# Kernel optimization log

Hardware: AMD Instinct MI355X
Metric: run time of the kernel (lower is better)

## Reference

```python
import jax, jax.numpy as jnp
import numpy as np

B, RATIO, IN_CH, H = 32, 32, 64, 8
E = IN_CH * H                 # embed_dim = in_channels * n_heads = 512
NODES_PER_GRAPH = 512
N = B * NODES_PER_GRAPH       # 16384 source nodes


def setup_inputs() -> dict:
    key = jax.random.key(0)
    ks = jax.random.split(key, 6)
    x = jax.random.normal(ks[0], (N, E), dtype=jnp.float32)
    # edge_index is accepted by forward but unused in 'attn' mode
    edge_index = jax.random.randint(ks[1], (2, 262144), 0, N, dtype=jnp.int32)
    # per-node graph id, sorted, equal-size graphs (batch[-1] + 1 == B)
    batch = jnp.repeat(jnp.arange(B, dtype=jnp.int32), NODES_PER_GRAPH)
    # learned params: cluster query seeds + MultiheadAttention in/out projections
    xcent_base = jax.random.normal(ks[2], (RATIO, E), dtype=jnp.float32)
    in_proj_w = jax.random.normal(ks[3], (3 * E, E), dtype=jnp.float32) / np.sqrt(E).astype(np.float32)
    in_proj_b = jnp.zeros((3 * E,), dtype=jnp.float32)
    out_proj_w = jax.random.normal(ks[4], (E, E), dtype=jnp.float32) / np.sqrt(E).astype(np.float32)
    out_proj_b = jnp.zeros((E,), dtype=jnp.float32)
    return dict(x=x, edge_index=edge_index, batch=batch, xcent_base=xcent_base,
                in_proj_w=in_proj_w, in_proj_b=in_proj_b,
                out_proj_w=out_proj_w, out_proj_b=out_proj_b)


def reference(x, edge_index, batch, xcent_base, in_proj_w, in_proj_b, out_proj_w, out_proj_b):
    # BipartPool.forward, mode='attn':
    #   x_aggrs = xcent_base.repeat(batch_size, 1)  -> queries [L, E], L = B*ratio
    #   MultiheadAttention(q=x_aggrs, k=v=x, attn_mask=mask[batch].T)
    # mask[batch].T is True (disallowed) where query's graph != node's graph.
    L = B * RATIO
    head_dim = E // H
    x_aggrs = jnp.tile(xcent_base, (B, 1))                        # [L, E]

    wq, wk, wv = jnp.split(in_proj_w, 3, axis=0)                  # each [E, E]
    bq, bk, bv = jnp.split(in_proj_b, 3, axis=0)
    q = (x_aggrs @ wq.T + bq).reshape(L, H, head_dim).transpose(1, 0, 2)  # [H, L, hd]
    k = (x @ wk.T + bk).reshape(N, H, head_dim).transpose(1, 0, 2)        # [H, N, hd]
    v = (x @ wv.T + bv).reshape(N, H, head_dim).transpose(1, 0, 2)        # [H, N, hd]

    batchcent = jnp.repeat(jnp.arange(B, dtype=batch.dtype), RATIO)       # [L]
    allowed = batchcent[:, None] == batch[None, :]                        # [L, N]

    scale = np.float32(1.0 / np.sqrt(head_dim))
    scores = jnp.einsum('hld,hnd->hln', q, k) * scale                     # [H, L, N]
    scores = jnp.where(allowed[None], scores, -jnp.inf)
    attn = jax.nn.softmax(scores, axis=-1)
    out = jnp.einsum('hln,hnd->hld', attn, v)                             # [H, L, hd]
    out = out.transpose(1, 0, 2).reshape(L, E)
    xcent = out @ out_proj_w.T + out_proj_b                               # [L, E]
    # original returns (xcent.reshape(B, ratio, E), None, None, batchcent, None, None)
    return xcent.reshape(B, RATIO, E), batchcent
```

## Files before the change

kernel.cpp:

```cpp
#include <hip/hip_runtime.h>
#include <hip/hip_bf16.h>

#define NGRAPH 32
#define NHEAD 8
#define EMB 512
#define NNODES 16384
#define NPG 512
#define LQ 1024
#define PST 520

typedef __attribute__((ext_vector_type(8))) short short8;
typedef __attribute__((ext_vector_type(4))) float f32x4;

static __device__ __forceinline__ unsigned short f2bf(float f) {
  union { float f; unsigned u; } v; v.f = f;
  unsigned r = (v.u + 0x7fffu + ((v.u >> 16) & 1u)) >> 16;
  return (unsigned short)r;
}

static __device__ __forceinline__ void gload_lds16(const ushort* g, ushort* l) {
  __builtin_amdgcn_global_load_lds(
      (const __attribute__((address_space(1))) unsigned*)g,
      (__attribute__((address_space(3))) unsigned*)l, 16, 0, 0);
}

#define BARRIER_LGKM()                                        \
  do {                                                        \
    asm volatile("s_waitcnt lgkmcnt(0)" ::: "memory");        \
    __builtin_amdgcn_s_barrier();                             \
  } while (0)

__global__ __launch_bounds__(256) void prep_x(const float* __restrict__ x,
                                              ushort* __restrict__ xb,
                                              ushort* __restrict__ xbT) {
  __shared__ ushort tile[64][68];
  int id = blockIdx.x;
  int xr = id & 7, j = id >> 3;
  int m = j >> 6, r = j & 63;
  int g = xr + 8 * m;
  int bc = r & 7;
  int br = g * 8 + (r >> 3);
  int t = threadIdx.x;
  int trr = t >> 4, tc = t & 15;
#pragma unroll
  for (int p = 0; p < 4; ++p) {
    int n = trr + p * 16;
    long gi = (long)(br * 64 + n) * EMB + bc * 64 + tc * 4;
    float4 v = *reinterpret_cast<const float4*>(x + gi);
    ushort4 o;
    o.x = f2bf(v.x); o.y = f2bf(v.y); o.z = f2bf(v.z); o.w = f2bf(v.w);
    *reinterpret_cast<ushort4*>(xb + gi) = o;
    *reinterpret_cast<ushort4*>(&tile[n][tc * 4]) = o;
  }
  __syncthreads();
#pragma unroll
  for (int p = 0; p < 4; ++p) {
    int e = trr + p * 16;
    int n0 = tc * 4;
    ushort4 o;
    o.x = tile[n0][e]; o.y = tile[n0 + 1][e];
    o.z = tile[n0 + 2][e]; o.w = tile[n0 + 3][e];
    *reinterpret_cast<ushort4*>(xbT + (long)(bc * 64 + e) * NNODES + br * 64 + n0) = o;
  }
}

__global__ void prep_wb(const float* __restrict__ wv, const float* __restrict__ wo,
                        const float* __restrict__ wq, const float* __restrict__ xc,
                        const float* __restrict__ wk,
                        ushort* __restrict__ wvb, ushort* __restrict__ wob,
                        ushort* __restrict__ wqb, ushort* __restrict__ xcb,
                        ushort* __restrict__ wkT, float* __restrict__ bcent) {
  __shared__ ushort tile[32][33];
  int b = blockIdx.x;
  if (b == 784) {
    int i = threadIdx.x;
#pragma unroll
    for (int p = 0; p < 4; ++p) bcent[i + p * 256] = (float)((i + p * 256) >> 5);
    return;
  }
  if (b >= 785) {
    int b2 = b - 785;
    int bd = b2 >> 4, bk = b2 & 15;
    int t = threadIdx.x, lr = t >> 5, lc = t & 31;
#pragma unroll
    for (int p = 0; p < 4; ++p) {
      int rr = lr + p * 8;
      tile[rr][lc] = f2bf(0.125f * wk[(long)(bd * 32 + rr) * EMB + bk * 32 + lc]);
    }
    __syncthreads();
#pragma unroll
    for (int p = 0; p < 4; ++p) {
      int rr = lr + p * 8;
      wkT[(long)(bk * 32 + rr) * EMB + bd * 32 + lc] = tile[lc][rr];
    }
    return;
  }
  const float* src; ushort* dst; int off;
  if (b < 256)       { src = wv; dst = wvb; off = b; }
  else if (b < 512)  { src = wo; dst = wob; off = b - 256; }
  else if (b < 768)  { src = wq; dst = wqb; off = b - 512; }
  else               { src = xc; dst = xcb; off = b - 768; }
  int i = (off * 256 + threadIdx.x) * 4;
  float4 v = *reinterpret_cast<const float4*>(src + i);
  ushort4 o;
  o.x = f2bf(v.x); o.y = f2bf(v.y); o.z = f2bf(v.z); o.w = f2bf(v.w);
  *reinterpret_cast<ushort4*>(dst + i) = o;
}

__global__ __launch_bounds__(256) void qpc_mfma(
    const ushort* __restrict__ xcb, const ushort* __restrict__ wqb,
    const float* __restrict__ bq, const ushort* __restrict__ wkTb,
    ushort* __restrict__ PCb) {
  __shared__ ushort Qs[32][72];
  int h = blockIdx.x >> 2, qs = blockIdx.x & 3;
  int t = threadIdx.x, w = t >> 6, lane = t & 63;
  int lr = lane & 15, grp = lane >> 4, ko = grp * 8;

  f32x4 qa[2];
  qa[0] = (f32x4)(0.0f); qa[1] = (f32x4)(0.0f);
#pragma unroll 4
  for (int kk = 0; kk < EMB; kk += 32) {
    short8 a0 = *reinterpret_cast<const short8*>(xcb + lr * EMB + kk + ko);
    short8 a1 = *reinterpret_cast<const short8*>(xcb + (16 + lr) * EMB + kk + ko);
    short8 b  = *reinterpret_cast<const short8*>(wqb + (long)(h * 64 + w * 16 + lr) * EMB + kk + ko);
    qa[0] = __builtin_amdgcn_mfma_f32_16x16x32_bf16(a0, b, qa[0], 0, 0, 0);
    qa[1] = __builtin_amdgcn_mfma_f32_16x16x32_bf16(a1, b, qa[1], 0, 0, 0);
  }
  float bias = bq[h * 64 + w * 16 + lr];
#pragma unroll
  for (int i = 0; i < 2; ++i)
#pragma unroll
    for (int r = 0; r < 4; ++r)
      Qs[i * 16 + grp * 4 + r][w * 16 + lr] = f2bf(qa[i][r] + bias);
  __syncthreads();

  f32x4 pa[2][2];
#pragma unroll
  for (int i = 0; i < 2; ++i)
#pragma unroll
    for (int j = 0; j < 2; ++j) pa[i][j] = (f32x4)(0.0f);
#pragma unroll
  for (int kk = 0; kk < 64; kk += 32) {
    short8 a0 = *reinterpret_cast<const short8*>(&Qs[lr][kk + ko]);
    short8 a1 = *reinterpret_cast<const short8*>(&Qs[16 + lr][kk + ko]);
#pragma unroll
    for (int j = 0; j < 2; ++j) {
      short8 b = *reinterpret_cast<const short8*>(
          wkTb + (long)(qs * 128 + w * 32 + j * 16 + lr) * EMB + h * 64 + kk + ko);
      pa[0][j] = __builtin_amdgcn_mfma_f32_16x16x32_bf16(a0, b, pa[0][j], 0, 0, 0);
      pa[1][j] = __builtin_amdgcn_mfma_f32_16x16x32_bf16(a1, b, pa[1][j], 0, 0, 0);
    }
  }
#pragma unroll
  for (int i = 0; i < 2; ++i)
#pragma unroll
    for (int j = 0; j < 2; ++j)
#pragma unroll
      for (int r = 0; r < 4; ++r)
        PCb[(long)(h * 32 + i * 16 + grp * 4 + r) * EMB + qs * 128 + w * 32 + j * 16 + lr] =
            f2bf(pa[i][j][r]);
}

__global__ __launch_bounds__(1024) void fused_attn(
    const ushort* __restrict__ PCb, const ushort* __restrict__ xb,
    const ushort* __restrict__ xbT, const ushort* __restrict__ wvb,
    const float* __restrict__ bvb, ushort* __restrict__ aout) {
  __shared__ ushort PCl[32 * PST];
  __shared__ ushort PBuf[32 * PST];
  __shared__ ushort Bbuf[2][16384];
  __shared__ float rmax[32][16];
  __shared__ float rsum[32][16];

  const int g = blockIdx.x & 31, h = blockIdx.x >> 5;
  const int t = threadIdx.x, w = t >> 6, lane = t & 63;
  const int lr = lane & 15, grp = lane >> 4;
  const int koU = grp * 8;

  const ushort* xg  = xb  + (long)g * NPG * EMB;
  const ushort* xTg = xbT + g * NPG;

  const int srow0 = w * 32 + (lane >> 2);
  const int spart = lane & 3;

  auto STAGE1 = [&](int c, int db) {
#pragma unroll
    for (int q = 0; q < 2; ++q) {
      int row = srow0 + q * 16;
      int psrc = spart ^ ((row >> 1) & 3);
      gload_lds16(xg + (long)row * EMB + c * 32 + psrc * 8,
                  &Bbuf[db][(w * 32 + q * 16) * 32]);
    }
  };
  auto STAGE3 = [&](int c, int db) {
#pragma unroll
    for (int q = 0; q < 2; ++q) {
      int row = srow0 + q * 16;
      int psrc = spart ^ ((row >> 1) & 3);
      gload_lds16(xTg + (long)row * NNODES + c * 32 + psrc * 8,
                  &Bbuf[db][(w * 32 + q * 16) * 32]);
    }
  };

  STAGE1(0, 0);
  STAGE1(1, 1);
  {
    const ushort* pc = PCb + h * 32 * EMB;
#pragma unroll
    for (int p = 0; p < 2; ++p) {
      int u = t + p * 1024;
      int row = u >> 6, col = (u & 63) * 8;
      *reinterpret_cast<short8*>(&PCl[row * PST + col]) =
          *reinterpret_cast<const short8*>(pc + row * EMB + col);
    }
  }
  BARRIER_LGKM();

  f32x4 acc[2][2];
#pragma unroll
  for (int i = 0; i < 2; ++i)
#pragma unroll
    for (int j = 0; j < 2; ++j) acc[i][j] = (f32x4)(0.0f);

#pragma unroll
  for (int c = 0; c < 16; ++c) {
    const int db = c & 1;
    asm volatile("s_waitcnt vmcnt(2)" ::: "memory");
    __builtin_amdgcn_sched_barrier(0);
    short8 a0 = *reinterpret_cast<const short8*>(&PCl[lr * PST + c * 32 + koU]);
    short8 a1 = *reinterpret_cast<const short8*>(&PCl[(16 + lr) * PST + c * 32 + koU]);
    short8 bv[2];
#pragma unroll
    for (int j = 0; j < 2; ++j) {
      int n = w * 32 + j * 16 + lr;
      int psrc = grp ^ ((n >> 1) & 3);
      bv[j] = *reinterpret_cast<const short8*>(&Bbuf[db][n * 32 + psrc * 8]);
    }
#pragma unroll
    for (int j = 0; j < 2; ++j) {
      acc[0][j] = __builtin_amdgcn_mfma_f32_16x16x32_bf16(a0, bv[j], acc[0][j], 0, 0, 0);
      acc[1][j] = __builtin_amdgcn_mfma_f32_16x16x32_bf16(a1, bv[j], acc[1][j], 0, 0, 0);
    }
    __builtin_amdgcn_sched_barrier(0);
    if (c < 14) STAGE1(c + 2, db);
    else        STAGE3(c - 14, db);
  }

#pragma unroll
  for (int i = 0; i < 2; ++i)
#pragma unroll
    for (int r = 0; r < 4; ++r) {
      float m = fmaxf(acc[i][0][r], acc[i][1][r]);
      m = fmaxf(m, __shfl_xor(m, 1)); m = fmaxf(m, __shfl_xor(m, 2));
      m = fmaxf(m, __shfl_xor(m, 4)); m = fmaxf(m, __shfl_xor(m, 8));
      if (lr == 0) rmax[i * 16 + grp * 4 + r][w] = m;
    }
  BARRIER_LGKM();
#pragma unroll
  for (int i = 0; i < 2; ++i)
#pragma unroll
    for (int r = 0; r < 4; ++r) {
      int row = i * 16 + grp * 4 + r;
      float m = rmax[row][0];
#pragma unroll
      for (int q = 1; q < 16; ++q) m = fmaxf(m, rmax[row][q]);
      float s = 0.f;
#pragma unroll
      for (int j = 0; j < 2; ++j) {
        float e = __expf(acc[i][j][r] - m);
        acc[i][j][r] = e;
        s += e;
      }
      s += __shfl_xor(s, 1); s += __shfl_xor(s, 2);
      s += __shfl_xor(s, 4); s += __shfl_xor(s, 8);
      if (lr == 0) rsum[row][w] = s;
    }
  BARRIER_LGKM();
#pragma unroll
  for (int i = 0; i < 2; ++i)
#pragma unroll
    for (int r = 0; r < 4; ++r) {
      int row = i * 16 + grp * 4 + r;
      float tot = rsum[row][0];
#pragma unroll
      for (int q = 1; q < 16; ++q) tot += rsum[row][q];
      float inv = 1.f / tot;
#pragma unroll
      for (int j = 0; j < 2; ++j)
        PBuf[row * PST + w * 32 + j * 16 + lr] = f2bf(acc[i][j][r] * inv);
    }
  BARRIER_LGKM();

  f32x4 acc2[2][2];
#pragma unroll
  for (int i = 0; i < 2; ++i)
#pragma unroll
    for (int j = 0; j < 2; ++j) acc2[i][j] = (f32x4)(0.0f);

#pragma unroll
  for (int c = 0; c < 16; ++c) {
    const int db = c & 1;
    if (c < 15) asm volatile("s_waitcnt vmcnt(2)" ::: "memory");
    else        asm volatile("s_waitcnt vmcnt(0)" ::: "memory");
    __builtin_amdgcn_sched_barrier(0);
    short8 a0 = *reinterpret_cast<const short8*>(&PBuf[lr * PST + c * 32 + koU]);
    short8 a1 = *reinterpret_cast<const short8*>(&PBuf[(16 + lr) * PST + c * 32 + koU]);
    short8 bv[2];
#pragma unroll
    for (int j = 0; j < 2; ++j) {
      int e = w * 32 + j * 16 + lr;
      int psrc = grp ^ ((e >> 1) & 3);
      bv[j] = *reinterpret_cast<const short8*>(&Bbuf[db][e * 32 + psrc * 8]);
    }
#pragma unroll
    for (int j = 0; j < 2; ++j) {
      acc2[0][j] = __builtin_amdgcn_mfma_f32_16x16x32_bf16(a0, bv[j], acc2[0][j], 0, 0, 0);
      acc2[1][j] = __builtin_amdgcn_mfma_f32_16x16x32_bf16(a1, bv[j], acc2[1][j], 0, 0, 0);
    }
    __builtin_amdgcn_sched_barrier(0);
    if (c < 14) STAGE3(c + 2, db);
  }
  BARRIER_LGKM();

#pragma unroll
  for (int i = 0; i < 2; ++i)
#pragma unroll
    for (int r = 0; r < 4; ++r) {
      int row = i * 16 + grp * 4 + r;
#pragma unroll
      for (int j = 0; j < 2; ++j)
        PBuf[row * PST + w * 32 + j * 16 + lr] = f2bf(acc2[i][j][r]);
    }
  BARRIER_LGKM();

  if (w < 8) {
    int wr = w >> 2, wc = w & 3;
    f32x4 acc3 = (f32x4)(0.0f);
    const ushort* wvh = wvb + (long)(h * 64 + wc * 16) * EMB;
#pragma unroll
    for (int c = 0; c < 16; ++c) {
      short8 a = *reinterpret_cast<const short8*>(&PBuf[(wr * 16 + lr) * PST + c * 32 + koU]);
      short8 b = *reinterpret_cast<const short8*>(wvh + (long)lr * EMB + c * 32 + koU);
      acc3 = __builtin_amdgcn_mfma_f32_16x16x32_bf16(a, b, acc3, 0, 0, 0);
    }
    float bias = bvb[h * 64 + wc * 16 + lr];
#pragma unroll
    for (int r = 0; r < 4; ++r) {
      int row = wr * 16 + grp * 4 + r;
      aout[(long)(g * 32 + row) * EMB + h * 64 + wc * 16 + lr] = f2bf(acc3[r] + bias);
    }
  }
}

template <int KK, int FM, int FN, int WM, int WN, bool OUT_BF16, bool HAS_BIAS>
__global__ void gemm_abt(const ushort* __restrict__ A, const ushort* __restrict__ Bm,
                         void* __restrict__ C, const float* __restrict__ bias,
                         int lda, int ldb, int ldc) {
  int tid = threadIdx.x;
  int wave = tid >> 6, lane = tid & 63;
  int wr = wave / WN, wc = wave % WN;
  int rowBase = blockIdx.y * (WM * FM * 16) + wr * FM * 16;
  int colBase = blockIdx.x * (WN * FN * 16) + wc * FN * 16;
  int lr = lane & 15;
  int ko = (lane >> 4) * 8;

  f32x4 acc[FM][FN];
#pragma unroll
  for (int i = 0; i < FM; ++i)
#pragma unroll
    for (int j = 0; j < FN; ++j) acc[i][j] = (f32x4)(0.0f);

#pragma unroll 8
  for (int kk = 0; kk < KK; kk += 32) {
    short8 av[FM], bv[FN];
#pragma unroll
    for (int i = 0; i < FM; ++i)
      av[i] = *reinterpret_cast<const short8*>(A + (long)(rowBase + i * 16 + lr) * lda + kk + ko);
#pragma unroll
    for (int j = 0; j < FN; ++j)
      bv[j] = *reinterpret_cast<const short8*>(Bm + (long)(colBase + j * 16 + lr) * ldb + kk + ko);
#pragma unroll
    for (int i = 0; i < FM; ++i)
#pragma unroll
      for (int j = 0; j < FN; ++j)
        acc[i][j] = __builtin_amdgcn_mfma_f32_16x16x32_bf16(av[i], bv[j], acc[i][j], 0, 0, 0);
  }

  int or0 = (lane >> 4) * 4;
#pragma unroll
  for (int i = 0; i < FM; ++i) {
#pragma unroll
    for (int j = 0; j < FN; ++j) {
      int col = colBase + j * 16 + lr;
      float bval = HAS_BIAS ? bias[col] : 0.f;
#pragma unroll
      for (int r = 0; r < 4; ++r) {
        int row = rowBase + i * 16 + or0 + r;
        float v = acc[i][j][r] + bval;
        if (OUT_BF16)
          ((ushort*)C)[(long)row * ldc + col] = f2bf(v);
        else
          ((float*)C)[(long)row * ldc + col] = v;
      }
    }
  }
}

extern "C" void kernel_launch(void* const* d_in, const int* in_sizes, int n_in,
                              void* d_out, int out_size, void* d_ws, size_t ws_size,
                              hipStream_t stream) {
  const float* x          = (const float*)d_in[0];
  const float* xcent_base = (const float*)d_in[3];
  const float* in_proj_w  = (const float*)d_in[4];
  const float* in_proj_b  = (const float*)d_in[5];
  const float* out_proj_w = (const float*)d_in[6];
  const float* out_proj_b = (const float*)d_in[7];

  char* w = (char*)d_ws;
  ushort* xb   = (ushort*)(w);
  ushort* xbT  = (ushort*)(w + 16777216);
  ushort* PCb  = (ushort*)(w + 33554432);
  ushort* wvb  = (ushort*)(w + 33816576);
  ushort* wob  = (ushort*)(w + 34340864);
  ushort* wqb  = (ushort*)(w + 34865152);
  ushort* wkTb = (ushort*)(w + 35389440);
  ushort* xcb  = (ushort*)(w + 35913728);
  ushort* aout = (ushort*)(w + 35946496);

  const float* wq = in_proj_w;
  const float* wk = in_proj_w + 512 * 512;
  const float* wv = in_proj_w + 1024 * 512;
  const float* bq = in_proj_b;
  const float* bv = in_proj_b + 1024;

  prep_x<<<2048, 256, 0, stream>>>(x, xb, xbT);
  prep_wb<<<1041, 256, 0, stream>>>(wv, out_proj_w, wq, xcent_base, wk,
                                    wvb, wob, wqb, xcb, wkTb,
                                    (float*)d_out + LQ * EMB);
  qpc_mfma<<<32, 256, 0, stream>>>(xcb, wqb, bq, wkTb, PCb);

  fused_attn<<<256, 1024, 0, stream>>>(PCb, xb, xbT, wvb, bv, aout);

  gemm_abt<512, 1, 2, 2, 2, false, true><<<dim3(8, 32, 1), 256, 0, stream>>>(
      aout, wob, d_out, out_proj_b, 512, 512, 512);
}
```

Baseline: 62.94 us.

## Fuse prep kernels and Q·Wk precompute; fold out-projection into attention via atomics

Merges the x conversion, weight conversion, batchcent fill and the Q/PC precompute into a single prep_all launch. The PC blocks now read fp32 weights directly, converting Wq and xcent inline and staging a transposed Wk slice in LDS. The separate out-projection GEMM is removed: each attention block multiplies its per-head output by the matching Wo slice and atomically adds into a zeroed fp32 output. This cuts launches and the aout round-trip, but adds a memset, fp32 atomics across 8 heads with non-deterministic summation order, and a serial tail in every attention block.

```diff
diff --git a/kernel.cpp b/kernel.cpp
--- a/kernel.cpp
+++ b/kernel.cpp
@@ -18,6 +18,13 @@
   return (unsigned short)r;
 }
 
+static __device__ __forceinline__ short8 cvt8(float4 a, float4 b) {
+  short8 r;
+  r[0] = f2bf(a.x); r[1] = f2bf(a.y); r[2] = f2bf(a.z); r[3] = f2bf(a.w);
+  r[4] = f2bf(b.x); r[5] = f2bf(b.y); r[6] = f2bf(b.z); r[7] = f2bf(b.w);
+  return r;
+}
+
 static __device__ __forceinline__ void gload_lds16(const ushort* g, ushort* l) {
   __builtin_amdgcn_global_load_lds(
       (const __attribute__((address_space(1))) unsigned*)g,
@@ -30,144 +37,151 @@
     __builtin_amdgcn_s_barrier();                             \
   } while (0)
 
-__global__ __launch_bounds__(256) void prep_x(const float* __restrict__ x,
-                                              ushort* __restrict__ xb,
-                                              ushort* __restrict__ xbT) {
-  __shared__ ushort tile[64][68];
-  int id = blockIdx.x;
-  int xr = id & 7, j = id >> 3;
-  int m = j >> 6, r = j & 63;
-  int g = xr + 8 * m;
-  int bc = r & 7;
-  int br = g * 8 + (r >> 3);
-  int t = threadIdx.x;
-  int trr = t >> 4, tc = t & 15;
-#pragma unroll
-  for (int p = 0; p < 4; ++p) {
-    int n = trr + p * 16;
-    long gi = (long)(br * 64 + n) * EMB + bc * 64 + tc * 4;
-    float4 v = *reinterpret_cast<const float4*>(x + gi);
+__global__ __launch_bounds__(256) void prep_all(
+    const float* __restrict__ x, const float* __restrict__ wv,
+    const float* __restrict__ wo, const float* __restrict__ wq,
+    const float* __restrict__ wk, const float* __restrict__ xc,
+    const float* __restrict__ bq,
+    ushort* __restrict__ xb, ushort* __restrict__ xbT,
+    ushort* __restrict__ wvb, ushort* __restrict__ wob,
+    ushort* __restrict__ PCb, float* __restrict__ bcent) {
+  __shared__ ushort smemU[11776];
+  const int b = blockIdx.x;
+  const int t = threadIdx.x;
+
+  if (b < 2048) {
+    ushort* tile = smemU;
+    int xr = b & 7, j = b >> 3;
+    int m = j >> 6, r = j & 63;
+    int g = xr + 8 * m;
+    int bc = r & 7;
+    int br = g * 8 + (r >> 3);
+    int trr = t >> 4, tc = t & 15;
+#pragma unroll
+    for (int p = 0; p < 4; ++p) {
+      int n = trr + p * 16;
+      long gi = (long)(br * 64 + n) * EMB + bc * 64 + tc * 4;
+      float4 v = *reinterpret_cast<const float4*>(x + gi);
+      ushort4 o;
+      o.x = f2bf(v.x); o.y = f2bf(v.y); o.z = f2bf(v.z); o.w = f2bf(v.w);
+      *reinterpret_cast<ushort4*>(xb + gi) = o;
+      *reinterpret_cast<ushort4*>(&tile[n * 68 + tc * 4]) = o;
+    }
+    __syncthreads();
+#pragma unroll
+    for (int p = 0; p < 4; ++p) {
+      int e = trr + p * 16;
+      int n0 = tc * 4;
+      ushort4 o;
+      o.x = tile[n0 * 68 + e];       o.y = tile[(n0 + 1) * 68 + e];
+      o.z = tile[(n0 + 2) * 68 + e]; o.w = tile[(n0 + 3) * 68 + e];
+      *reinterpret_cast<ushort4*>(xbT + (long)(bc * 64 + e) * NNODES + br * 64 + n0) = o;
+    }
+    return;
+  }
+
+  if (b < 2560) {
+    int off = b - 2048;
+    const float* src = (off < 256) ? wv : wo;
+    ushort* dst = (off < 256) ? wvb : wob;
+    off &= 255;
+    int i = (off * 256 + t) * 4;
+    float4 v = *reinterpret_cast<const float4*>(src + i);
     ushort4 o;
     o.x = f2bf(v.x); o.y = f2bf(v.y); o.z = f2bf(v.z); o.w = f2bf(v.w);
-    *reinterpret_cast<ushort4*>(xb + gi) = o;
-    *reinterpret_cast<ushort4*>(&tile[n][tc * 4]) = o;
-  }
-  __syncthreads();
-#pragma unroll
-  for (int p = 0; p < 4; ++p) {
-    int e = trr + p * 16;
-    int n0 = tc * 4;
-    ushort4 o;
-    o.x = tile[n0][e]; o.y = tile[n0 + 1][e];
-    o.z = tile[n0 + 2][e]; o.w = tile[n0 + 3][e];
-    *reinterpret_cast<ushort4*>(xbT + (long)(bc * 64 + e) * NNODES + br * 64 + n0) = o;
-  }
-}
-
-__global__ void prep_wb(const float* __restrict__ wv, const float* __restrict__ wo,
-                        const float* __restrict__ wq, const float* __restrict__ xc,
-                        const float* __restrict__ wk,
-                        ushort* __restrict__ wvb, ushort* __restrict__ wob,
-                        ushort* __restrict__ wqb, ushort* __restrict__ xcb,
-                        ushort* __restrict__ wkT, float* __restrict__ bcent) {
-  __shared__ ushort tile[32][33];
-  int b = blockIdx.x;
-  if (b == 784) {
-    int i = threadIdx.x;
-#pragma unroll
-    for (int p = 0; p < 4; ++p) bcent[i + p * 256] = (float)((i + p * 256) >> 5);
+    *reinterpret_cast<ushort4*>(dst + i) = o;
     return;
   }
-  if (b >= 785) {
-    int b2 = b - 785;
-    int bd = b2 >> 4, bk = b2 & 15;
-    int t = threadIdx.x, lr = t >> 5, lc = t & 31;
-#pragma unroll
-    for (int p = 0; p < 4; ++p) {
-      int rr = lr + p * 8;
-      tile[rr][lc] = f2bf(0.125f * wk[(long)(bd * 32 + rr) * EMB + bk * 32 + lc]);
-    }
+
+  if (b == 2560) {
+#pragma unroll
+    for (int p = 0; p < 4; ++p) bcent[t + p * 256] = (float)((t + p * 256) >> 5);
+    return;
+  }
+
+  {
+    ushort* Qs  = smemU;
+    ushort* WkT = smemU + 2304;
+    int qb = b - 2561;
+    int h = qb >> 2, qs = qb & 3;
+    int w = t >> 6, lane = t & 63;
+    int lr = lane & 15, grp = lane >> 4, ko = grp * 8;
+
+    {
+      int dl = t >> 2, cq = t & 3;
+      const float* wr = wk + (long)(h * 64 + dl) * EMB + qs * 128;
+#pragma unroll
+      for (int m = 0; m < 8; ++m) {
+        int c0 = cq * 32 + m * 4;
+        float4 v = *reinterpret_cast<const float4*>(wr + c0);
+        WkT[(c0 + 0) * 72 + dl] = f2bf(0.125f * v.x);
+        WkT[(c0 + 1) * 72 + dl] = f2bf(0.125f * v.y);
+        WkT[(c0 + 2) * 72 + dl] = f2bf(0.125f * v.z);
+        WkT[(c0 + 3) * 72 + dl] = f2bf(0.125f * v.w);
+      }
+    }
+
+    f32x4 qa[2];
+    qa[0] = (f32x4)(0.0f); qa[1] = (f32x4)(0.0f);
+#pragma unroll 4
+    for (int kk = 0; kk < EMB; kk += 32) {
+      const float* xr0 = xc + lr * EMB + kk + ko;
+      const float* xr1 = xc + (16 + lr) * EMB + kk + ko;
+      const float* wr  = wq + (long)(h * 64 + w * 16 + lr) * EMB + kk + ko;
+      short8 a0 = cvt8(*reinterpret_cast<const float4*>(xr0),
+                       *reinterpret_cast<const float4*>(xr0 + 4));
+      short8 a1 = cvt8(*reinterpret_cast<const float4*>(xr1),
+                       *reinterpret_cast<const float4*>(xr1 + 4));
+      short8 bb = cvt8(*reinterpret_cast<const float4*>(wr),
+                       *reinterpret_cast<const float4*>(wr + 4));
+      qa[0] = __builtin_amdgcn_mfma_f32_16x16x32_bf16(a0, bb, qa[0], 0, 0, 0);
+      qa[1] = __builtin_amdgcn_mfma_f32_16x16x32_bf16(a1, bb, qa[1], 0, 0, 0);
+    }
+    float bias = bq[h * 64 + w * 16 + lr];
+#pragma unroll
+    for (int i = 0; i < 2; ++i)
+#pragma unroll
+      for (int r = 0; r < 4; ++r)
+        Qs[(i * 16 + grp * 4 + r) * 72 + w * 16 + lr] = f2bf(qa[i][r] + bias);
     __syncthreads();
-#pragma unroll
-    for (int p = 0; p < 4; ++p) {
-      int rr = lr + p * 8;
-      wkT[(long)(bk * 32 + rr) * EMB + bd * 32 + lc] = tile[lc][rr];
-    }
-    return;
-  }
-  const float* src; ushort* dst; int off;
-  if (b < 256)       { src = wv; dst = wvb; off = b; }
-  else if (b < 512)  { src = wo; dst = wob; off = b - 256; }
-  else if (b < 768)  { src = wq; dst = wqb; off = b - 512; }
-  else               { src = xc; dst = xcb; off = b - 768; }
-  int i = (off * 256 + threadIdx.x) * 4;
-  float4 v = *reinterpret_cast<const float4*>(src + i);
-  ushort4 o;
-  o.x = f2bf(v.x); o.y = f2bf(v.y); o.z = f2bf(v.z); o.w = f2bf(v.w);
-  *reinterpret_cast<ushort4*>(dst + i) = o;
-}
-
-__global__ __launch_bounds__(256) void qpc_mfma(
-    const ushort* __restrict__ xcb, const ushort* __restrict__ wqb,
-    const float* __restrict__ bq, const ushort* __restrict__ wkTb,
-    ushort* __restrict__ PCb) {
-  __shared__ ushort Qs[32][72];
-  int h = blockIdx.x >> 2, qs = blockIdx.x & 3;
-  int t = threadIdx.x, w = t >> 6, lane = t & 63;
-  int lr = lane & 15, grp = lane >> 4, ko = grp * 8;
-
-  f32x4 qa[2];
-  qa[0] = (f32x4)(0.0f); qa[1] = (f32x4)(0.0f);
-#pragma unroll 4
-  for (int kk = 0; kk < EMB; kk += 32) {
-    short8 a0 = *reinterpret_cast<const short8*>(xcb + lr * EMB + kk + ko);
-    short8 a1 = *reinterpret_cast<const short8*>(xcb + (16 + lr) * EMB + kk + ko);
-    short8 b  = *reinterpret_cast<const short8*>(wqb + (long)(h * 64 + w * 16 + lr) * EMB + kk + ko);
-    qa[0] = __builtin_amdgcn_mfma_f32_16x16x32_bf16(a0, b, qa[0], 0, 0, 0);
-    qa[1] = __builtin_amdgcn_mfma_f32_16x16x32_bf16(a1, b, qa[1], 0, 0, 0);
-  }
-  float bias = bq[h * 64 + w * 16 + lr];
-#pragma unroll
-  for (int i = 0; i < 2; ++i)
-#pragma unroll
-    for (int r = 0; r < 4; ++r)
-      Qs[i * 16 + grp * 4 + r][w * 16 + lr] = f2bf(qa[i][r] + bias);
-  __syncthreads();
-
-  f32x4 pa[2][2];
-#pragma unroll
-  for (int i = 0; i < 2; ++i)
-#pragma unroll
-    for (int j = 0; j < 2; ++j) pa[i][j] = (f32x4)(0.0f);
-#pragma unroll
-  for (int kk = 0; kk < 64; kk += 32) {
-    short8 a0 = *reinterpret_cast<const short8*>(&Qs[lr][kk + ko]);
-    short8 a1 = *reinterpret_cast<const short8*>(&Qs[16 + lr][kk + ko]);
-#pragma unroll
-    for (int j = 0; j < 2; ++j) {
-      short8 b = *reinterpret_cast<const short8*>(
-          wkTb + (long)(qs * 128 + w * 32 + j * 16 + lr) * EMB + h * 64 + kk + ko);
-      pa[0][j] = __builtin_amdgcn_mfma_f32_16x16x32_bf16(a0, b, pa[0][j], 0, 0, 0);
-      pa[1][j] = __builtin_amdgcn_mfma_f32_16x16x32_bf16(a1, b, pa[1][j], 0, 0, 0);
-    }
-  }
-#pragma unroll
-  for (int i = 0; i < 2; ++i)
-#pragma unroll
-    for (int j = 0; j < 2; ++j)
-#pragma unroll
-      for (int r = 0; r < 4; ++r)
-        PCb[(long)(h * 32 + i * 16 + grp * 4 + r) * EMB + qs * 128 + w * 32 + j * 16 + lr] =
-            f2bf(pa[i][j][r]);
+
+    f32x4 pa[2][2];
+#pragma unroll
+    for (int i = 0; i < 2; ++i)
+#pragma unroll
+      for (int j = 0; j < 2; ++j) pa[i][j] = (f32x4)(0.0f);
+#pragma unroll
+    for (int kk = 0; kk < 64; kk += 32) {
+      short8 a0 = *reinterpret_cast<const short8*>(&Qs[lr * 72 + kk + ko]);
+      short8 a1 = *reinterpret_cast<const short8*>(&Qs[(16 + lr) * 72 + kk + ko]);
+#pragma unroll
+      for (int j = 0; j < 2; ++j) {
+        short8 bb = *reinterpret_cast<const short8*>(
+            &WkT[(w * 32 + j * 16 + lr) * 72 + kk + ko]);
+        pa[0][j] = __builtin_amdgcn_mfma_f32_16x16x32_bf16(a0, bb, pa[0][j], 0, 0, 0);
+        pa[1][j] = __builtin_amdgcn_mfma_f32_16x16x32_bf16(a1, bb, pa[1][j], 0, 0, 0);
+      }
+    }
+#pragma unroll
+    for (int i = 0; i < 2; ++i)
+#pragma unroll
+      for (int j = 0; j < 2; ++j)
+#pragma unroll
+        for (int r = 0; r < 4; ++r)
+          PCb[(long)(h * 32 + i * 16 + grp * 4 + r) * EMB + qs * 128 + w * 32 + j * 16 + lr] =
+              f2bf(pa[i][j][r]);
+  }
 }
 
 __global__ __launch_bounds__(1024) void fused_attn(
     const ushort* __restrict__ PCb, const ushort* __restrict__ xb,
     const ushort* __restrict__ xbT, const ushort* __restrict__ wvb,
-    const float* __restrict__ bvb, ushort* __restrict__ aout) {
+    const ushort* __restrict__ wob, const float* __restrict__ bvb,
+    const float* __restrict__ bob, float* __restrict__ outf) {
   __shared__ ushort PCl[32 * PST];
   __shared__ ushort PBuf[32 * PST];
   __shared__ ushort Bbuf[2][16384];
+  __shared__ ushort aoutS[32 * 72];
   __shared__ float rmax[32][16];
   __shared__ float rsum[32][16];
 
@@ -228,17 +242,17 @@
     __builtin_amdgcn_sched_barrier(0);
     short8 a0 = *reinterpret_cast<const short8*>(&PCl[lr * PST + c * 32 + koU]);
     short8 a1 = *reinterpret_cast<const short8*>(&PCl[(16 + lr) * PST + c * 32 + koU]);
-    short8 bv[2];
+    short8 bv8[2];
 #pragma unroll
     for (int j = 0; j < 2; ++j) {
       int n = w * 32 + j * 16 + lr;
       int psrc = grp ^ ((n >> 1) & 3);
-      bv[j] = *reinterpret_cast<const short8*>(&Bbuf[db][n * 32 + psrc * 8]);
-    }
-#pragma unroll
-    for (int j = 0; j < 2; ++j) {
-      acc[0][j] = __builtin_amdgcn_mfma_f32_16x16x32_bf16(a0, bv[j], acc[0][j], 0, 0, 0);
-      acc[1][j] = __builtin_amdgcn_mfma_f32_16x16x32_bf16(a1, bv[j], acc[1][j], 0, 0, 0);
+      bv8[j] = *reinterpret_cast<const short8*>(&Bbuf[db][n * 32 + psrc * 8]);
+    }
+#pragma unroll
+    for (int j = 0; j < 2; ++j) {
+      acc[0][j] = __builtin_amdgcn_mfma_f32_16x16x32_bf16(a0, bv8[j], acc[0][j], 0, 0, 0);
+      acc[1][j] = __builtin_amdgcn_mfma_f32_16x16x32_bf16(a1, bv8[j], acc[1][j], 0, 0, 0);
     }
     __builtin_amdgcn_sched_barrier(0);
     if (c < 14) STAGE1(c + 2, db);
@@ -304,17 +318,17 @@
     __builtin_amdgcn_sched_barrier(0);
     short8 a0 = *reinterpret_cast<const short8*>(&PBuf[lr * PST + c * 32 + koU]);
     short8 a1 = *reinterpret_cast<const short8*>(&PBuf[(16 + lr) * PST + c * 32 + koU]);
-    short8 bv[2];
+    short8 bv8[2];
 #pragma unroll
     for (int j = 0; j < 2; ++j) {
       int e = w * 32 + j * 16 + lr;
       int psrc = grp ^ ((e >> 1) & 3);
-      bv[j] = *reinterpret_cast<const short8*>(&Bbuf[db][e * 32 + psrc * 8]);
-    }
-#pragma unroll
-    for (int j = 0; j < 2; ++j) {
-      acc2[0][j] = __builtin_amdgcn_mfma_f32_16x16x32_bf16(a0, bv[j], acc2[0][j], 0, 0, 0);
-      acc2[1][j] = __builtin_amdgcn_mfma_f32_16x16x32_bf16(a1, bv[j], acc2[1][j], 0, 0, 0);
+      bv8[j] = *reinterpret_cast<const short8*>(&Bbuf[db][e * 32 + psrc * 8]);
+    }
+#pragma unroll
+    for (int j = 0; j < 2; ++j) {
+      acc2[0][j] = __builtin_amdgcn_mfma_f32_16x16x32_bf16(a0, bv8[j], acc2[0][j], 0, 0, 0);
+      acc2[1][j] = __builtin_amdgcn_mfma_f32_16x16x32_bf16(a1, bv8[j], acc2[1][j], 0, 0, 0);
     }
     __builtin_amdgcn_sched_barrier(0);
     if (c < 14) STAGE3(c + 2, db);
@@ -346,63 +360,40 @@
 #pragma unroll
     for (int r = 0; r < 4; ++r) {
       int row = wr * 16 + grp * 4 + r;
-      aout[(long)(g * 32 + row) * EMB + h * 64 + wc * 16 + lr] = f2bf(acc3[r] + bias);
-    }
-  }
-}
-
-template <int KK, int FM, int FN, int WM, int WN, bool OUT_BF16, bool HAS_BIAS>
-__global__ void gemm_abt(const ushort* __restrict__ A, const ushort* __restrict__ Bm,
-                         void* __restrict__ C, const float* __restrict__ bias,
-                         int lda, int ldb, int ldc) {
-  int tid = threadIdx.x;
-  int wave = tid >> 6, lane = tid & 63;
-  int wr = wave / WN, wc = wave % WN;
-  int rowBase = blockIdx.y * (WM * FM * 16) + wr * FM * 16;
-  int colBase = blockIdx.x * (WN * FN * 16) + wc * FN * 16;
-  int lr = lane & 15;
-  int ko = (lane >> 4) * 8;
-
-  f32x4 acc[FM][FN];
-#pragma unroll
-  for (int i = 0; i < FM; ++i)
-#pragma unroll
-    for (int j = 0; j < FN; ++j) acc[i][j] = (f32x4)(0.0f);
-
-#pragma unroll 8
-  for (int kk = 0; kk < KK; kk += 32) {
-    short8 av[FM], bv[FN];
-#pragma unroll
-    for (int i = 0; i < FM; ++i)
-      av[i] = *reinterpret_cast<const short8*>(A + (long)(rowBase + i * 16 + lr) * lda + kk + ko);
-#pragma unroll
-    for (int j = 0; j < FN; ++j)
-      bv[j] = *reinterpret_cast<const short8*>(Bm + (long)(colBase + j * 16 + lr) * ldb + kk + ko);
-#pragma unroll
-    for (int i = 0; i < FM; ++i)
-#pragma unroll
-      for (int j = 0; j < FN; ++j)
-        acc[i][j] = __builtin_amdgcn_mfma_f32_16x16x32_bf16(av[i], bv[j], acc[i][j], 0, 0, 0);
-  }
-
-  int or0 = (lane >> 4) * 4;
-#pragma unroll
-  for (int i = 0; i < FM; ++i) {
-#pragma unroll
-    for (int j = 0; j < FN; ++j) {
-      int col = colBase + j * 16 + lr;
-      float bval = HAS_BIAS ? bias[col] : 0.f;
+      aoutS[row * 72 + wc * 16 + lr] = f2bf(acc3[r] + bias);
+    }
+  }
+  BARRIER_LGKM();
+
+  f32x4 acc4[2][2];
+#pragma unroll
+  for (int i = 0; i < 2; ++i)
+#pragma unroll
+    for (int j = 0; j < 2; ++j) acc4[i][j] = (f32x4)(0.0f);
+#pragma unroll
+  for (int kk = 0; kk < 64; kk += 32) {
+    short8 a0 = *reinterpret_cast<const short8*>(&aoutS[lr * 72 + kk + koU]);
+    short8 a1 = *reinterpret_cast<const short8*>(&aoutS[(16 + lr) * 72 + kk + koU]);
+#pragma unroll
+    for (int j = 0; j < 2; ++j) {
+      short8 bb = *reinterpret_cast<const short8*>(
+          wob + (long)(w * 32 + j * 16 + lr) * EMB + h * 64 + kk + koU);
+      acc4[0][j] = __builtin_amdgcn_mfma_f32_16x16x32_bf16(a0, bb, acc4[0][j], 0, 0, 0);
+      acc4[1][j] = __builtin_amdgcn_mfma_f32_16x16x32_bf16(a1, bb, acc4[1][j], 0, 0, 0);
+    }
+  }
+#pragma unroll
+  for (int i = 0; i < 2; ++i)
+#pragma unroll
+    for (int j = 0; j < 2; ++j) {
+      int col = w * 32 + j * 16 + lr;
+      float bias = (h == 0) ? bob[col] : 0.f;
 #pragma unroll
       for (int r = 0; r < 4; ++r) {
-        int row = rowBase + i * 16 + or0 + r;
-        float v = acc[i][j][r] + bval;
-        if (OUT_BF16)
-          ((ushort*)C)[(long)row * ldc + col] = f2bf(v);
-        else
-          ((float*)C)[(long)row * ldc + col] = v;
+        int row = g * 32 + i * 16 + grp * 4 + r;
+        unsafeAtomicAdd(&outf[(long)row * EMB + col], acc4[i][j][r] + bias);
       }
     }
-  }
 }
 
 extern "C" void kernel_launch(void* const* d_in, const int* in_sizes, int n_in,
@@ -421,10 +412,6 @@
   ushort* PCb  = (ushort*)(w + 33554432);
   ushort* wvb  = (ushort*)(w + 33816576);
   ushort* wob  = (ushort*)(w + 34340864);
-  ushort* wqb  = (ushort*)(w + 34865152);
-  ushort* wkTb = (ushort*)(w + 35389440);
-  ushort* xcb  = (ushort*)(w + 35913728);
-  ushort* aout = (ushort*)(w + 35946496);
 
   const float* wq = in_proj_w;
   const float* wk = in_proj_w + 512 * 512;
@@ -432,14 +419,12 @@
   const float* bq = in_proj_b;
   const float* bv = in_proj_b + 1024;
 
-  prep_x<<<2048, 256, 0, stream>>>(x, xb, xbT);
-  prep_wb<<<1041, 256, 0, stream>>>(wv, out_proj_w, wq, xcent_base, wk,
-                                    wvb, wob, wqb, xcb, wkTb,
-                                    (float*)d_out + LQ * EMB);
-  qpc_mfma<<<32, 256, 0, stream>>>(xcb, wqb, bq, wkTb, PCb);
-
-  fused_attn<<<256, 1024, 0, stream>>>(PCb, xb, xbT, wvb, bv, aout);
-
-  gemm_abt<512, 1, 2, 2, 2, false, true><<<dim3(8, 32, 1), 256, 0, stream>>>(
-      aout, wob, d_out, out_proj_b, 512, 512, 512);
-}
+  hipMemsetAsync(d_out, 0, (size_t)LQ * EMB * sizeof(float), stream);
+
+  prep_all<<<2593, 256, 0, stream>>>(x, wv, out_proj_w, wq, wk, xcent_base, bq,
+                                     xb, xbT, wvb, wob, PCb,
+                                     (float*)d_out + (long)LQ * EMB);
+
+  fused_attn<<<256, 1024, 0, stream>>>(PCb, xb, xbT, wvb, wob, bv, out_proj_b,
+                                       (float*)d_out);
+}
```

After: 80.01 us. +27.1%, slower.
